# Optimization experiments

Measured on AMD Instinct MI355X. Metric: run time of the kernel, lower is better.

## Reference

```python
import jax, jax.numpy as jnp
import numpy as np

D_MODEL, N_HEAD, HEAD_SIZE = 1024, 16, 64
NEG_INF = -1e30


def setup_inputs() -> dict:
    key = jax.random.key(0)
    ks = jax.random.split(key, 12)
    B, S = 4, 4096
    w = 0.02
    return {
        "query": jax.random.normal(ks[0], (B, S, D_MODEL), jnp.float32),
        "key":   jax.random.normal(ks[1], (B, S, D_MODEL), jnp.float32),
        "value": jax.random.normal(ks[2], (B, S, D_MODEL), jnp.float32),
        "mask":  jnp.ones((HEAD_SIZE, HEAD_SIZE), jnp.int32),
        "Wq": jax.random.normal(ks[3], (D_MODEL, HEAD_SIZE), jnp.float32) * w,
        "bq": jnp.zeros((HEAD_SIZE,), jnp.float32),
        "Wk": jax.random.normal(ks[4], (D_MODEL, HEAD_SIZE), jnp.float32) * w,
        "bk": jnp.zeros((HEAD_SIZE,), jnp.float32),
        "Wv": jax.random.normal(ks[5], (D_MODEL, HEAD_SIZE), jnp.float32) * w,
        "bv": jnp.zeros((HEAD_SIZE,), jnp.float32),
        "Wp": jax.random.normal(ks[6], (D_MODEL, D_MODEL), jnp.float32) * w,
        "bp": jnp.zeros((D_MODEL,), jnp.float32),
    }


def reference(query, key, value, mask, Wq, bq, Wk, bk, Wv, bv, Wp, bp):
    h, dh = N_HEAD, HEAD_SIZE
    # Linear projections: (B,S,d_model) -> (B,S,head_size)
    q = query @ Wq + bq
    k = key @ Wk + bk
    v = value @ Wv + bv
    # Faithful to torch: view(-1, h, dh).transpose(1,2) on (B,S,head_size)
    # -> (N, dh, h) with N = B*S/h
    q = q.reshape(-1, h, dh).transpose(0, 2, 1)
    k = k.reshape(-1, h, dh).transpose(0, 2, 1)
    v = v.reshape(-1, h, dh).transpose(0, 2, 1)
    scale = q.shape[-1] ** (-0.5)  # dhead = h in the original code
    # scores: (N, dh, dh)
    scores = jnp.einsum('nik,njk->nij', q, k) * scale
    scores = jnp.where(mask == 0, NEG_INF, scores)
    # NOTE: original code computes softmax(scores) but then overwrites it;
    # the actual output uses dropout(raw scores) @ v. Dropout in eval = identity.
    x = jnp.einsum('nij,njh->nih', scores, v)  # (N, dh, h)
    x = x.transpose(0, 2, 1).reshape(-1, h * dh)  # (N, d_model)
    return x @ Wp + bp
```

## Files before the change

kernel.cpp:

```cpp
#include <hip/hip_runtime.h>
#include <hip/hip_bf16.h>
#include <stdint.h>


typedef float f32x4 __attribute__((ext_vector_type(4)));
typedef short s16x8 __attribute__((ext_vector_type(8)));

#define T_TOK 16384
#define KDIM  1024
#define HS    64

__device__ __forceinline__ short f2bf(float f) {
    union { float f; uint32_t u; } x; x.f = f;
    uint32_t u = x.u;
    u += 0x7FFFu + ((u >> 16) & 1u);
    return (short)(u >> 16);
}

__global__ __launch_bounds__(256) void wtrans_kernel(
    const float* __restrict__ Wq, const float* __restrict__ Wk,
    const float* __restrict__ Wv, const float* __restrict__ Wp,
    short* __restrict__ Wtq, short* __restrict__ Wtk,
    short* __restrict__ Wtv, short* __restrict__ Wpt)
{
    const int bid = blockIdx.x;
    const float* src; short* dst; int N, k0, n0;
    if (bid < 256) { src = Wp; dst = Wpt; N = 1024; k0 = (bid >> 4) * 64; n0 = (bid & 15) * 64; }
    else {
        int r = bid - 256; int p = r >> 4;
        src = (p == 0) ? Wq : (p == 1) ? Wk : Wv;
        dst = (p == 0) ? Wtq : (p == 1) ? Wtk : Wtv;
        N = 64; k0 = (r & 15) * 64; n0 = 0;
    }
    __shared__ float Ts[64][68];
    const int tid = threadIdx.x;
    #pragma unroll
    for (int i = 0; i < 4; ++i) {
        int idx = i * 256 + tid;
        int r = idx >> 4, c4 = idx & 15;
        f32x4 v = *(const f32x4*)&src[(size_t)(k0 + r) * N + n0 + c4 * 4];
        *(f32x4*)&Ts[r][c4 * 4] = v;
    }
    __syncthreads();
    #pragma unroll
    for (int i = 0; i < 2; ++i) {
        int idx = i * 256 + tid;
        int n = idx >> 3, c8 = idx & 7;
        s16x8 h;
        #pragma unroll
        for (int j = 0; j < 8; ++j) h[j] = f2bf(Ts[c8 * 8 + j][n]);
        *(s16x8*)&dst[(size_t)(n0 + n) * KDIM + k0 + c8 * 8] = h;
    }
}

__global__ __launch_bounds__(256) void qkv_proj_kernel(
    const float* __restrict__ Q, const float* __restrict__ K,
    const float* __restrict__ V,
    const short* __restrict__ Wtq, const short* __restrict__ Wtk,
    const short* __restrict__ Wtv,
    const float* __restrict__ bq, const float* __restrict__ bk,
    const float* __restrict__ bv,
    float* __restrict__ OutQKV)
{
    const int p = blockIdx.y;
    const int z = blockIdx.z;
    const float* In = (p == 0) ? Q : (p == 1) ? K : V;
    const short* Wt = (p == 0) ? Wtq : (p == 1) ? Wtk : Wtv;
    const float* bb = (p == 0) ? bq : (p == 1) ? bk : bv;
    float* Out = OutQKV + ((size_t)z * 3 + p) * T_TOK * HS;

    const int tid  = threadIdx.x;
    const int wave = tid >> 6;
    const int lane = tid & 63;
    const int lhi  = lane >> 4;
    const int llo  = lane & 15;
    const int t0   = blockIdx.x * 64;
    const int kb   = z * 512;

    const float* Ap = In + (size_t)(t0 + wave * 16 + llo) * KDIM + kb + lhi * 8;
    const short* Bp = Wt + (size_t)llo * KDIM + kb + lhi * 8;

    f32x4 acc[4] = {};

    #pragma unroll
    for (int c = 0; c < 8; ++c) {
        const int k0 = c * 64;
        f32x4 a0l = *(const f32x4*)(Ap + k0);
        f32x4 a0h = *(const f32x4*)(Ap + k0 + 4);
        f32x4 a1l = *(const f32x4*)(Ap + k0 + 32);
        f32x4 a1h = *(const f32x4*)(Ap + k0 + 36);
        s16x8 bfr[2][4];
        #pragma unroll
        for (int hh = 0; hh < 2; ++hh)
            #pragma unroll
            for (int nb = 0; nb < 4; ++nb)
                bfr[hh][nb] = *(const s16x8*)(Bp + (size_t)nb * 16 * KDIM + k0 + hh * 32);
        s16x8 af0, af1;
        af0[0] = f2bf(a0l.x); af0[1] = f2bf(a0l.y); af0[2] = f2bf(a0l.z); af0[3] = f2bf(a0l.w);
        af0[4] = f2bf(a0h.x); af0[5] = f2bf(a0h.y); af0[6] = f2bf(a0h.z); af0[7] = f2bf(a0h.w);
        af1[0] = f2bf(a1l.x); af1[1] = f2bf(a1l.y); af1[2] = f2bf(a1l.z); af1[3] = f2bf(a1l.w);
        af1[4] = f2bf(a1h.x); af1[5] = f2bf(a1h.y); af1[6] = f2bf(a1h.z); af1[7] = f2bf(a1h.w);
        #pragma unroll
        for (int nb = 0; nb < 4; ++nb)
            acc[nb] = __builtin_amdgcn_mfma_f32_16x16x32_bf16(af0, bfr[0][nb], acc[nb], 0, 0, 0);
        #pragma unroll
        for (int nb = 0; nb < 4; ++nb)
            acc[nb] = __builtin_amdgcn_mfma_f32_16x16x32_bf16(af1, bfr[1][nb], acc[nb], 0, 0, 0);
    }

    #pragma unroll
    for (int nb = 0; nb < 4; ++nb) {
        const float bias = (z == 0) ? bb[nb * 16 + llo] : 0.0f;
        #pragma unroll
        for (int r = 0; r < 4; ++r)
            Out[(size_t)(t0 + wave * 16 + lhi * 4 + r) * HS + nb * 16 + llo] = acc[nb][r] + bias;
    }
}

__global__ __launch_bounds__(256) void group_attn_kernel(
    const float* __restrict__ QKV, short* __restrict__ Xbf)
{
    const int n = blockIdx.x;
    __shared__ float Sq[16][68];
    __shared__ float Sk[16][68];
    __shared__ float Sv[16][68];
    __shared__ float KV[16][17];

    const int tid = threadIdx.x;
    const size_t zoff = (size_t)3 * T_TOK * HS;
    const float* qp = QKV + (size_t)n * 16 * HS;
    const float* kp = qp + (size_t)T_TOK * HS;
    const float* vp = kp + (size_t)T_TOK * HS;

    {
        int row = tid >> 4, c4 = (tid & 15) * 4;
        f32x4 q0 = *(const f32x4*)&qp[tid * 4];
        f32x4 q1 = *(const f32x4*)&qp[zoff + tid * 4];
        f32x4 k0 = *(const f32x4*)&kp[tid * 4];
        f32x4 k1 = *(const f32x4*)&kp[zoff + tid * 4];
        f32x4 v0 = *(const f32x4*)&vp[tid * 4];
        f32x4 v1 = *(const f32x4*)&vp[zoff + tid * 4];
        *(f32x4*)&Sq[row][c4] = q0 + q1;
        *(f32x4*)&Sk[row][c4] = k0 + k1;
        *(f32x4*)&Sv[row][c4] = v0 + v1;
    }
    __syncthreads();

    {
        int b = tid >> 4, a = tid & 15;
        const f32x4* kb = (const f32x4*)&Sk[b][0];
        const f32x4* va = (const f32x4*)&Sv[a][0];
        float s = 0.f;
        #pragma unroll
        for (int j = 0; j < 16; ++j) {
            f32x4 x = kb[j], y = va[j];
            s += x.x * y.x + x.y * y.y + x.z * y.z + x.w * y.w;
        }
        KV[b][a] = s * 0.25f;
    }
    __syncthreads();

    const int i = tid & 63;
    const int w = tid >> 6;
    float qv[16];
    #pragma unroll
    for (int b = 0; b < 16; ++b) qv[b] = Sq[b][i];
    #pragma unroll
    for (int u = 0; u < 4; ++u) {
        int a = u * 4 + w;
        float s = 0.f;
        #pragma unroll
        for (int b = 0; b < 16; ++b) s += qv[b] * KV[b][a];
        Xbf[(size_t)n * 1024 + a * 64 + i] = f2bf(s);
    }
}

__global__ __launch_bounds__(256) void out_proj_kernel(
    const short* __restrict__ Xbf, const short* __restrict__ Wpt,
    const float* __restrict__ bp, float* __restrict__ Out)
{
    const int tid  = threadIdx.x;
    const int wave = tid >> 6;
    const int lane = tid & 63;
    const int lhi  = lane >> 4, llo = lane & 15;
    const int n0   = blockIdx.x * 32 + (wave & 1) * 16;
    const int m0   = blockIdx.y * 32 + (wave >> 1) * 16;

    const short* Ap = Xbf + (size_t)(m0 + llo) * KDIM + lhi * 8;
    const short* Bp = Wpt + (size_t)(n0 + llo) * KDIM + lhi * 8;

    f32x4 acc = {};

    #pragma unroll
    for (int c = 0; c < 16; ++c) {
        const int k0 = c * 64;
        s16x8 af0 = *(const s16x8*)(Ap + k0);
        s16x8 af1 = *(const s16x8*)(Ap + k0 + 32);
        s16x8 bf0 = *(const s16x8*)(Bp + k0);
        s16x8 bf1 = *(const s16x8*)(Bp + k0 + 32);
        acc = __builtin_amdgcn_mfma_f32_16x16x32_bf16(af0, bf0, acc, 0, 0, 0);
        acc = __builtin_amdgcn_mfma_f32_16x16x32_bf16(af1, bf1, acc, 0, 0, 0);
    }

    const float bias = bp[n0 + llo];
    #pragma unroll
    for (int r = 0; r < 4; ++r)
        Out[(size_t)(m0 + lhi * 4 + r) * KDIM + n0 + llo] = acc[r] + bias;
}

extern "C" void kernel_launch(void* const* d_in, const int* in_sizes, int n_in,
                              void* d_out, int out_size, void* d_ws, size_t ws_size,
                              hipStream_t stream) {
    const float* Q  = (const float*)d_in[0];
    const float* K  = (const float*)d_in[1];
    const float* V  = (const float*)d_in[2];
    const float* Wq = (const float*)d_in[4];
    const float* bq = (const float*)d_in[5];
    const float* Wk = (const float*)d_in[6];
    const float* bk = (const float*)d_in[7];
    const float* Wv = (const float*)d_in[8];
    const float* bv = (const float*)d_in[9];
    const float* Wp = (const float*)d_in[10];
    const float* bp = (const float*)d_in[11];
    float* out = (float*)d_out;

    char* ws = (char*)d_ws;
    float* qkv = (float*)ws;
    size_t off = (size_t)2 * 3 * T_TOK * HS * sizeof(float);
    short* Xbf = (short*)(ws + off); off += (size_t)1024 * 1024 * 2;
    short* Wtq = (short*)(ws + off); off += (size_t)HS * KDIM * 2;
    short* Wtk = (short*)(ws + off); off += (size_t)HS * KDIM * 2;
    short* Wtv = (short*)(ws + off); off += (size_t)HS * KDIM * 2;
    short* Wpt = (short*)(ws + off); off += (size_t)KDIM * KDIM * 2;

    wtrans_kernel<<<dim3(304), 256, 0, stream>>>(Wq, Wk, Wv, Wp, Wtq, Wtk, Wtv, Wpt);
    qkv_proj_kernel<<<dim3(T_TOK / 64, 3, 2), 256, 0, stream>>>(
        Q, K, V, Wtq, Wtk, Wtv, bq, bk, bv, qkv);
    group_attn_kernel<<<dim3(1024), 256, 0, stream>>>(qkv, Xbf);
    out_proj_kernel<<<dim3(32, 32), 256, 0, stream>>>(Xbf, Wpt, bp, out);
}
```

Before: 281.3 us.

## Stage QKV input tile in swizzled LDS and drop split-K partial sums

The QKV projection now reads a 32-token by full-K fp32 input tile with coalesced 64-byte-per-lane loads, converts it to bf16, and stores it in an XOR-swizzled shared-memory tile. Each wave then computes one 16-column output slice over the full K dimension, reading A fragments from LDS. This removes the two-way split-K, so the attention kernel no longer reads and adds two partial QKV buffers and the workspace shrinks. In exchange each block uses 64 KB of LDS, which limits occupancy, and there is fewer blocks' worth of K-parallelism per token.

```diff
diff --git a/kernel.cpp b/kernel.cpp
--- a/kernel.cpp
+++ b/kernel.cpp
@@ -63,58 +63,72 @@
     float* __restrict__ OutQKV)
 {
     const int p = blockIdx.y;
-    const int z = blockIdx.z;
     const float* In = (p == 0) ? Q : (p == 1) ? K : V;
     const short* Wt = (p == 0) ? Wtq : (p == 1) ? Wtk : Wtv;
     const float* bb = (p == 0) ? bq : (p == 1) ? bk : bv;
-    float* Out = OutQKV + ((size_t)z * 3 + p) * T_TOK * HS;
+    float* Out = OutQKV + (size_t)p * T_TOK * HS;
+
+    __shared__ short Al[32 * 1024];
 
     const int tid  = threadIdx.x;
     const int wave = tid >> 6;
     const int lane = tid & 63;
     const int lhi  = lane >> 4;
     const int llo  = lane & 15;
-    const int t0   = blockIdx.x * 64;
-    const int kb   = z * 512;
-
-    const float* Ap = In + (size_t)(t0 + wave * 16 + llo) * KDIM + kb + lhi * 8;
-    const short* Bp = Wt + (size_t)llo * KDIM + kb + lhi * 8;
-
-    f32x4 acc[4] = {};
-
-    #pragma unroll
-    for (int c = 0; c < 8; ++c) {
-        const int k0 = c * 64;
-        f32x4 a0l = *(const f32x4*)(Ap + k0);
-        f32x4 a0h = *(const f32x4*)(Ap + k0 + 4);
-        f32x4 a1l = *(const f32x4*)(Ap + k0 + 32);
-        f32x4 a1h = *(const f32x4*)(Ap + k0 + 36);
-        s16x8 bfr[2][4];
-        #pragma unroll
-        for (int hh = 0; hh < 2; ++hh)
+    const int t0   = blockIdx.x * 32;
+
+    {
+        const float* rp = In + (size_t)(t0 + wave * 8) * KDIM + lane * 16;
+        f32x4 r0[8];
+        #pragma unroll
+        for (int rr = 0; rr < 8; ++rr)
+            r0[rr] = *(const f32x4*)(rp + (size_t)rr * KDIM);
+        #pragma unroll
+        for (int rr = 0; rr < 8; ++rr) {
+            const float* q = rp + (size_t)rr * KDIM;
+            f32x4 a1 = *(const f32x4*)(q + 4);
+            f32x4 a2 = *(const f32x4*)(q + 8);
+            f32x4 a3 = *(const f32x4*)(q + 12);
+            s16x8 h0, h1;
+            h0[0] = f2bf(r0[rr].x); h0[1] = f2bf(r0[rr].y); h0[2] = f2bf(r0[rr].z); h0[3] = f2bf(r0[rr].w);
+            h0[4] = f2bf(a1.x);     h0[5] = f2bf(a1.y);     h0[6] = f2bf(a1.z);     h0[7] = f2bf(a1.w);
+            h1[0] = f2bf(a2.x);     h1[1] = f2bf(a2.y);     h1[2] = f2bf(a2.z);     h1[3] = f2bf(a2.w);
+            h1[4] = f2bf(a3.x);     h1[5] = f2bf(a3.y);     h1[6] = f2bf(a3.z);     h1[7] = f2bf(a3.w);
+            const int row = wave * 8 + rr;
+            const int g0  = (2 * lane)     ^ (row & 7);
+            const int g1  = (2 * lane + 1) ^ (row & 7);
+            *(s16x8*)&Al[row * 1024 + g0 * 8] = h0;
+            *(s16x8*)&Al[row * 1024 + g1 * 8] = h1;
+        }
+    }
+    __syncthreads();
+
+    const short* Bp = Wt + (size_t)(wave * 16 + llo) * KDIM + lhi * 8;
+    f32x4 acc[2] = {};
+
+    #pragma unroll
+    for (int c = 0; c < 16; ++c) {
+        s16x8 b0 = *(const s16x8*)(Bp + c * 64);
+        s16x8 b1 = *(const s16x8*)(Bp + c * 64 + 32);
+        #pragma unroll
+        for (int hh = 0; hh < 2; ++hh) {
+            s16x8 bf = hh ? b1 : b0;
             #pragma unroll
-            for (int nb = 0; nb < 4; ++nb)
-                bfr[hh][nb] = *(const s16x8*)(Bp + (size_t)nb * 16 * KDIM + k0 + hh * 32);
-        s16x8 af0, af1;
-        af0[0] = f2bf(a0l.x); af0[1] = f2bf(a0l.y); af0[2] = f2bf(a0l.z); af0[3] = f2bf(a0l.w);
-        af0[4] = f2bf(a0h.x); af0[5] = f2bf(a0h.y); af0[6] = f2bf(a0h.z); af0[7] = f2bf(a0h.w);
-        af1[0] = f2bf(a1l.x); af1[1] = f2bf(a1l.y); af1[2] = f2bf(a1l.z); af1[3] = f2bf(a1l.w);
-        af1[4] = f2bf(a1h.x); af1[5] = f2bf(a1h.y); af1[6] = f2bf(a1h.z); af1[7] = f2bf(a1h.w);
-        #pragma unroll
-        for (int nb = 0; nb < 4; ++nb)
-            acc[nb] = __builtin_amdgcn_mfma_f32_16x16x32_bf16(af0, bfr[0][nb], acc[nb], 0, 0, 0);
-        #pragma unroll
-        for (int nb = 0; nb < 4; ++nb)
-            acc[nb] = __builtin_amdgcn_mfma_f32_16x16x32_bf16(af1, bfr[1][nb], acc[nb], 0, 0, 0);
-    }
-
-    #pragma unroll
-    for (int nb = 0; nb < 4; ++nb) {
-        const float bias = (z == 0) ? bb[nb * 16 + llo] : 0.0f;
+            for (int tt = 0; tt < 2; ++tt) {
+                const int row = tt * 16 + llo;
+                const int g   = c * 8 + ((hh * 4 + lhi) ^ (row & 7));
+                s16x8 af = *(const s16x8*)&Al[row * 1024 + g * 8];
+                acc[tt] = __builtin_amdgcn_mfma_f32_16x16x32_bf16(af, bf, acc[tt], 0, 0, 0);
+            }
+        }
+    }
+
+    const float bias = bb[wave * 16 + llo];
+    #pragma unroll
+    for (int tt = 0; tt < 2; ++tt)
         #pragma unroll
         for (int r = 0; r < 4; ++r)
-            Out[(size_t)(t0 + wave * 16 + lhi * 4 + r) * HS + nb * 16 + llo] = acc[nb][r] + bias;
-    }
+            Out[(size_t)(t0 + tt * 16 + lhi * 4 + r) * HS + wave * 16 + llo] = acc[tt][r] + bias;
 }
 
 __global__ __launch_bounds__(256) void group_attn_kernel(
@@ -127,22 +141,15 @@
     __shared__ float KV[16][17];
 
     const int tid = threadIdx.x;
-    const size_t zoff = (size_t)3 * T_TOK * HS;
     const float* qp = QKV + (size_t)n * 16 * HS;
     const float* kp = qp + (size_t)T_TOK * HS;
     const float* vp = kp + (size_t)T_TOK * HS;
 
     {
         int row = tid >> 4, c4 = (tid & 15) * 4;
-        f32x4 q0 = *(const f32x4*)&qp[tid * 4];
-        f32x4 q1 = *(const f32x4*)&qp[zoff + tid * 4];
-        f32x4 k0 = *(const f32x4*)&kp[tid * 4];
-        f32x4 k1 = *(const f32x4*)&kp[zoff + tid * 4];
-        f32x4 v0 = *(const f32x4*)&vp[tid * 4];
-        f32x4 v1 = *(const f32x4*)&vp[zoff + tid * 4];
-        *(f32x4*)&Sq[row][c4] = q0 + q1;
-        *(f32x4*)&Sk[row][c4] = k0 + k1;
-        *(f32x4*)&Sv[row][c4] = v0 + v1;
+        *(f32x4*)&Sq[row][c4] = *(const f32x4*)&qp[tid * 4];
+        *(f32x4*)&Sk[row][c4] = *(const f32x4*)&kp[tid * 4];
+        *(f32x4*)&Sv[row][c4] = *(const f32x4*)&vp[tid * 4];
     }
     __syncthreads();
 
@@ -226,7 +233,7 @@
 
     char* ws = (char*)d_ws;
     float* qkv = (float*)ws;
-    size_t off = (size_t)2 * 3 * T_TOK * HS * sizeof(float);
+    size_t off = (size_t)3 * T_TOK * HS * sizeof(float);
     short* Xbf = (short*)(ws + off); off += (size_t)1024 * 1024 * 2;
     short* Wtq = (short*)(ws + off); off += (size_t)HS * KDIM * 2;
     short* Wtk = (short*)(ws + off); off += (size_t)HS * KDIM * 2;
@@ -234,7 +241,7 @@
     short* Wpt = (short*)(ws + off); off += (size_t)KDIM * KDIM * 2;
 
     wtrans_kernel<<<dim3(304), 256, 0, stream>>>(Wq, Wk, Wv, Wp, Wtq, Wtk, Wtv, Wpt);
-    qkv_proj_kernel<<<dim3(T_TOK / 64, 3, 2), 256, 0, stream>>>(
+    qkv_proj_kernel<<<dim3(T_TOK / 32, 3), 256, 0, stream>>>(
         Q, K, V, Wtq, Wtk, Wtv, bq, bk, bv, qkv);
     group_attn_kernel<<<dim3(1024), 256, 0, stream>>>(qkv, Xbf);
     out_proj_kernel<<<dim3(32, 32), 256, 0, stream>>>(Xbf, Wpt, bp, out);
```

Measured after the change: 265.1 us. 1.06x faster.
